# Optimization experiments

Measured on AMD Instinct MI355X. Metric: run time of the kernel, lower is better.

## Reference

```python
import jax, jax.numpy as jnp
import numpy as np

IN_DIM = 64
B, C, H, W = 4, IN_DIM, 64, 64
KEY_CH = IN_DIM // 8  # softmax scale channel count (as in torch code)


def conv1x1(x, w, b):
    # x: [B,C,H,W], w: [O,C], b: [O] -> [B,O,H,W]
    return jnp.einsum('bchw,oc->bohw', x, w) + b[None, :, None, None]


def setup_inputs() -> dict:
    key = jax.random.key(0)
    ks = jax.random.split(key, 24)
    s = 0.05
    d16, d4 = IN_DIM // 16, IN_DIM // 4
    inp = {
        'input1': jax.random.normal(ks[0], (B, C, H, W), jnp.float32),
        'input2': jax.random.normal(ks[1], (B, C, H, W), jnp.float32),
        'wq1': jax.random.normal(ks[2], (d16, C), jnp.float32) * s,
        'bq1': jax.random.normal(ks[3], (d16,), jnp.float32) * s,
        'wq2': jax.random.normal(ks[4], (d16, C), jnp.float32) * s,
        'bq2': jax.random.normal(ks[5], (d16,), jnp.float32) * s,
        'wq3': jax.random.normal(ks[6], (d16, C), jnp.float32) * s,
        'bq3': jax.random.normal(ks[7], (d16,), jnp.float32) * s,
        'wq4': jax.random.normal(ks[8], (d16, C), jnp.float32) * s,
        'bq4': jax.random.normal(ks[9], (d16,), jnp.float32) * s,
        'wk': jax.random.normal(ks[10], (d4, C), jnp.float32) * s,
        'bk': jax.random.normal(ks[11], (d4,), jnp.float32) * s,
        'wv': jax.random.normal(ks[12], (C, C), jnp.float32) * s,
        'bv': jax.random.normal(ks[13], (C,), jnp.float32) * s,
        'wk2': jax.random.normal(ks[14], (d4, C), jnp.float32) * s,
        'bk2': jax.random.normal(ks[15], (d4,), jnp.float32) * s,
        'wv2': jax.random.normal(ks[16], (C, C), jnp.float32) * s,
        'bv2': jax.random.normal(ks[17], (C,), jnp.float32) * s,
        'gamma': jax.random.normal(ks[18], (1,), jnp.float32) * 0.1,
    }
    return inp


def _branch(q_in, feat, wk_, bk_, wv_, bv_, gamma, resid):
    b, c, h, w = feat.shape
    n = h * w
    scale = KEY_CH ** (-0.5)
    q = q_in.reshape(b, -1, n).transpose(0, 2, 1)            # [B,N,C/4]
    k = conv1x1(feat, wk_, bk_).reshape(b, -1, n)            # [B,C/4,N]
    attn = jax.nn.softmax(scale * jnp.einsum('bnd,bdm->bnm', q, k), axis=-1)  # [B,N,N]
    v = conv1x1(feat, wv_, bv_).reshape(b, c, n)             # [B,C,N]
    out = jnp.einsum('bcn,bmn->bcm', v, attn).reshape(b, c, h, w)
    return gamma[0] * out + resid


def reference(input1, input2, wq1, bq1, wq2, bq2, wq3, bq3, wq4, bq4,
              wk, bk, wv, bv, wk2, bk2, wv2, bv2, gamma):
    input3 = input1 + (input2 - input1) / 3
    input4 = input3 + (input2 - input1) / 3
    q1 = conv1x1(input1, wq1, bq1)
    q2 = conv1x1(input2, wq2, bq2)
    q3 = conv1x1(input3, wq3, bq3)
    q4 = conv1x1(input4, wq4, bq4)
    q_in1 = jnp.concatenate([q1, q3, q4, q2], axis=1)  # [B,C/4,H,W]
    q_in2 = jnp.concatenate([q2, q4, q3, q1], axis=1)
    out1 = _branch(q_in1, input1, wk, bk, wv, bv, gamma, input1)
    out2 = _branch(q_in2, input2, wk2, bk2, wv2, bv2, gamma, input2)
    return out1, out2
```

## Files before the change

kernel.cpp:

```cpp
#include <hip/hip_runtime.h>
#include <hip/hip_bf16.h>
#include <stdint.h>

typedef short bf16x8 __attribute__((ext_vector_type(8)));
typedef float f32x4  __attribute__((ext_vector_type(4)));
typedef float f32x16 __attribute__((ext_vector_type(16)));
typedef unsigned int u32;

#define N_SP 4096
#define QSCALE 0.5100697284f

__device__ inline unsigned short f2bf(float f) {
    unsigned u = __float_as_uint(f);
    u += 0x7fff + ((u >> 16) & 1);
    return (unsigned short)(u >> 16);
}
__device__ inline float bf2f(short s) {
    return __uint_as_float(((unsigned)(unsigned short)s) << 16);
}
__device__ inline u32 cvtpk_bf16(float lo, float hi) {
    u32 r;
    asm("v_cvt_pk_bf16_f32 %0, %1, %2" : "=v"(r) : "v"(lo), "v"(hi));
    return r;
}
__device__ inline void pl32swap(u32& a, u32& b) {
    asm volatile("v_permlane32_swap_b32 %0, %1" : "+v"(a), "+v"(b));
}


__global__ __launch_bounds__(256) void stage1_kernel(
    const float* __restrict__ in1, const float* __restrict__ in2,
    const float* __restrict__ wq1, const float* __restrict__ bq1,
    const float* __restrict__ wq2, const float* __restrict__ bq2,
    const float* __restrict__ wq3, const float* __restrict__ bq3,
    const float* __restrict__ wq4, const float* __restrict__ bq4,
    const float* __restrict__ wk,  const float* __restrict__ bk,
    const float* __restrict__ wv,  const float* __restrict__ bv,
    const float* __restrict__ wk2, const float* __restrict__ bk2,
    const float* __restrict__ wv2, const float* __restrict__ bv2,
    unsigned short* __restrict__ Qs, unsigned short* __restrict__ Ks,
    unsigned short* __restrict__ Vs)
{
    __shared__ unsigned short w1h[16][64];
    __shared__ unsigned short w2h[16][64];
    __shared__ unsigned short wkh[16][64];
    __shared__ unsigned short wvh[64][64];
    __shared__ float qb[16], kbb[16], vbb[64];

    const int bid = blockIdx.x;
    const int br = bid & 7;
    const int ntl = bid >> 3;
    const int b = br >> 1, rr = br & 1;
    const int tid = threadIdx.x;

    const float* wqs[4]; const float* bqs[4]; float c1s[4], c2s[4];
    if (rr == 0) {
        wqs[0]=wq1; bqs[0]=bq1; c1s[0]=1.f;       c2s[0]=0.f;
        wqs[1]=wq3; bqs[1]=bq3; c1s[1]=2.f/3.f;   c2s[1]=1.f/3.f;
        wqs[2]=wq4; bqs[2]=bq4; c1s[2]=1.f/3.f;   c2s[2]=2.f/3.f;
        wqs[3]=wq2; bqs[3]=bq2; c1s[3]=0.f;       c2s[3]=1.f;
    } else {
        wqs[0]=wq2; bqs[0]=bq2; c1s[0]=0.f;       c2s[0]=1.f;
        wqs[1]=wq4; bqs[1]=bq4; c1s[1]=1.f/3.f;   c2s[1]=2.f/3.f;
        wqs[2]=wq3; bqs[2]=bq3; c1s[2]=2.f/3.f;   c2s[2]=1.f/3.f;
        wqs[3]=wq1; bqs[3]=bq1; c1s[3]=1.f;       c2s[3]=0.f;
    }
    const float* wkp = rr ? wk2 : wk;  const float* bkp = rr ? bk2 : bk;
    const float* wvp = rr ? wv2 : wv;  const float* bvp = rr ? bv2 : bv;

    for (int e = tid; e < 1024; e += 256) {
        int g = e >> 8;
        int h = e >> 6;
        int ch = e & 63;
        float wq_ = wqs[g][e & 255];
        w1h[h][ch] = f2bf(c1s[g] * wq_ * QSCALE);
        w2h[h][ch] = f2bf(c2s[g] * wq_ * QSCALE);
        wkh[h][ch] = f2bf(wkp[e]);
    }
    for (int e = tid; e < 4096; e += 256) wvh[e >> 6][e & 63] = f2bf(wvp[e]);
    if (tid < 16) { qb[tid] = bqs[tid >> 2][tid & 3] * QSCALE; kbb[tid] = bkp[tid]; }
    if (tid < 64) vbb[tid] = bvp[tid];
    __syncthreads();

    const int nl = tid & 31;
    const int og = tid >> 5;
    const int n = ntl * 32 + nl;
    const float* x1p = in1 + (size_t)b * 64 * N_SP + n;
    const float* x2p = in2 + (size_t)b * 64 * N_SP + n;
    const float* xfp = rr ? x2p : x1p;

    if (og < 2) {
        float acc[8];
        #pragma unroll
        for (int o = 0; o < 8; o++) acc[o] = qb[og * 8 + o];
        for (int g = 0; g < 8; g++) {
            float x1v[8], x2v[8];
            #pragma unroll
            for (int cc = 0; cc < 8; cc++) {
                x1v[cc] = x1p[(size_t)(g * 8 + cc) * N_SP];
                x2v[cc] = x2p[(size_t)(g * 8 + cc) * N_SP];
            }
            #pragma unroll
            for (int o = 0; o < 8; o++) {
                bf16x8 w1v = *(const bf16x8*)(&w1h[og * 8 + o][g * 8]);
                bf16x8 w2v = *(const bf16x8*)(&w2h[og * 8 + o][g * 8]);
                #pragma unroll
                for (int cc = 0; cc < 8; cc++)
                    acc[o] += bf2f(w1v[cc]) * x1v[cc] + bf2f(w2v[cc]) * x2v[cc];
            }
        }
        bf16x8 qv;
        #pragma unroll
        for (int o = 0; o < 8; o++) qv[o] = (short)f2bf(acc[o]);
        *(bf16x8*)(Qs + (size_t)br * 65536 + ntl * 512 + og * 256 + nl * 8) = qv;
    } else if (og < 4) {
        const int dg = og - 2;
        float acc[8];
        #pragma unroll
        for (int o = 0; o < 8; o++) acc[o] = kbb[dg * 8 + o];
        for (int g = 0; g < 8; g++) {
            float xfv[8];
            #pragma unroll
            for (int cc = 0; cc < 8; cc++) xfv[cc] = xfp[(size_t)(g * 8 + cc) * N_SP];
            #pragma unroll
            for (int o = 0; o < 8; o++) {
                bf16x8 wkv = *(const bf16x8*)(&wkh[dg * 8 + o][g * 8]);
                #pragma unroll
                for (int cc = 0; cc < 8; cc++)
                    acc[o] += bf2f(wkv[cc]) * xfv[cc];
            }
        }
        bf16x8 kv;
        #pragma unroll
        for (int o = 0; o < 8; o++) kv[o] = (short)f2bf(acc[o]);
        *(bf16x8*)(Ks + (size_t)br * 65536 + ntl * 512 + nl * 16 + dg * 8) = kv;
    } else {
        const int cg = og - 4;
        float acc[16];
        #pragma unroll
        for (int j = 0; j < 16; j++) acc[j] = vbb[cg * 16 + j];
        for (int g = 0; g < 8; g++) {
            float xfv[8];
            #pragma unroll
            for (int cc = 0; cc < 8; cc++) xfv[cc] = xfp[(size_t)(g * 8 + cc) * N_SP];
            #pragma unroll
            for (int j = 0; j < 16; j++) {
                bf16x8 wvv = *(const bf16x8*)(&wvh[cg * 16 + j][g * 8]);
                #pragma unroll
                for (int cc = 0; cc < 8; cc++)
                    acc[j] += bf2f(wvv[cc]) * xfv[cc];
            }
        }
        size_t basen = (size_t)br * 262144 + (size_t)(n >> 5) * 2048 +
                       (size_t)((n >> 4) & 1) * 1024 + (size_t)((n >> 3) & 1) * 256 +
                       (n & 7);
        #pragma unroll
        for (int j = 0; j < 16; j++) {
            int c = cg * 16 + j;
            Vs[basen + (c >> 5) * 512 + (c & 31) * 8] = f2bf(acc[j]);
        }
    }
}

__global__ __launch_bounds__(256, 4) void attn_kernel(
    const unsigned short* __restrict__ Qs, const unsigned short* __restrict__ Ks,
    const unsigned short* __restrict__ Vs,
    const float* __restrict__ in1, const float* __restrict__ in2,
    const float* __restrict__ gamma_p, float* __restrict__ out)
{
    __shared__ float accb[4][64][33];
    __shared__ float rsl[4][32];
    __shared__ float invl[32];

    const int bid = blockIdx.x;
    const int br = bid & 7;
    const int qt = bid >> 3;
    const int b = br >> 1, rr = br & 1;
    const int tid = threadIdx.x;
    const int ks = tid >> 6;
    const int l = tid & 63;
    const int q31 = l & 31, hi = l >> 5;

    const unsigned short* Qb = Qs + (size_t)br * 65536;
    const unsigned short* Kb = Ks + (size_t)br * 65536;
    const unsigned short* Vb = Vs + (size_t)br * 262144;

    const bf16x8 aq = *(const bf16x8*)(Qb + qt * 512 + l * 8);

    f32x16 accA = {0,0,0,0,0,0,0,0,0,0,0,0,0,0,0,0};
    f32x16 accB = {0,0,0,0,0,0,0,0,0,0,0,0,0,0,0,0};
    float rsum = 0.f;

    const int koff = q31 * 16 + hi * 8;

    bf16x8 kf[2];
    bf16x8 vf[2][4];
    {
        const unsigned short* kp = Kb + (size_t)(ks * 32) * 512;
        const unsigned short* vp = Vb + (size_t)(ks * 32) * 2048;
        kf[0] = *(const bf16x8*)(kp + koff);
        #pragma unroll
        for (int j = 0; j < 4; j++) vf[0][j] = *(const bf16x8*)(vp + j * 512 + l * 8);
    }

    #pragma unroll
    for (int t = 0; t < 32; ++t) {
        const int cur = t & 1, nxt = cur ^ 1;
        const int tn = (t < 31) ? t + 1 : 31;
        {
            const unsigned short* kpn = Kb + (size_t)(ks * 32 + tn) * 512;
            const unsigned short* vpn = Vb + (size_t)(ks * 32 + tn) * 2048;
            kf[nxt] = *(const bf16x8*)(kpn + koff);
            #pragma unroll
            for (int j = 0; j < 4; j++) vf[nxt][j] = *(const bf16x8*)(vpn + j * 512 + l * 8);
        }

        const f32x16 z16 = {0,0,0,0,0,0,0,0,0,0,0,0,0,0,0,0};
        f32x16 s = __builtin_amdgcn_mfma_f32_32x32x16_bf16(kf[cur], aq, z16, 0, 0, 0);

        float p[16];
        #pragma unroll
        for (int r2 = 0; r2 < 16; ++r2) {
            p[r2] = exp2f(s[r2]);
            rsum += p[r2];
        }

        u32 a0 = cvtpk_bf16(p[0], p[1]);   u32 a2 = cvtpk_bf16(p[4], p[5]);
        pl32swap(a0, a2);
        u32 a1 = cvtpk_bf16(p[2], p[3]);   u32 a3 = cvtpk_bf16(p[6], p[7]);
        pl32swap(a1, a3);
        u32 c0 = cvtpk_bf16(p[8], p[9]);   u32 c2 = cvtpk_bf16(p[12], p[13]);
        pl32swap(c0, c2);
        u32 c1 = cvtpk_bf16(p[10], p[11]); u32 c3 = cvtpk_bf16(p[14], p[15]);
        pl32swap(c1, c3);

        union U { u32 w[4]; bf16x8 v; };
        U u0; u0.w[0] = a0; u0.w[1] = a1; u0.w[2] = a2; u0.w[3] = a3;
        U u1; u1.w[0] = c0; u1.w[1] = c1; u1.w[2] = c2; u1.w[3] = c3;

        accA = __builtin_amdgcn_mfma_f32_32x32x16_bf16(u0.v, vf[cur][0], accA, 0, 0, 0);
        accB = __builtin_amdgcn_mfma_f32_32x32x16_bf16(u0.v, vf[cur][1], accB, 0, 0, 0);
        accA = __builtin_amdgcn_mfma_f32_32x32x16_bf16(u1.v, vf[cur][2], accA, 0, 0, 0);
        accB = __builtin_amdgcn_mfma_f32_32x32x16_bf16(u1.v, vf[cur][3], accB, 0, 0, 0);
    }

    rsum += __shfl_xor(rsum, 32, 64);
    if (l < 32) rsl[ks][l] = rsum;

    #pragma unroll
    for (int r2 = 0; r2 < 16; ++r2) {
        int qrow = (r2 & 3) + 8 * (r2 >> 2) + 4 * hi;
        accb[ks][q31][qrow]      = accA[r2];
        accb[ks][32 + q31][qrow] = accB[r2];
    }
    __syncthreads();

    if (tid < 32)
        invl[tid] = 1.0f / (rsl[0][tid] + rsl[1][tid] + rsl[2][tid] + rsl[3][tid]);
    __syncthreads();

    const float g = gamma_p[0];
    const int c = tid >> 2, mg = tid & 3;
    const float* fp = (rr ? in2 : in1) + (size_t)b * 64 * N_SP + (size_t)c * N_SP +
                      qt * 32 + mg * 8;
    float* op = out + (size_t)rr * (4ull * 64 * N_SP) + (size_t)b * 64 * N_SP +
                (size_t)c * N_SP + qt * 32 + mg * 8;

    float ov[8];
    #pragma unroll
    for (int i = 0; i < 8; i++) {
        int q = mg * 8 + i;
        ov[i] = (accb[0][c][q] + accb[1][c][q] + accb[2][c][q] + accb[3][c][q]) * invl[q];
    }
    f32x4 f0 = *(const f32x4*)fp;
    f32x4 f1 = *(const f32x4*)(fp + 4);
    f32x4 o0, o1;
    #pragma unroll
    for (int i = 0; i < 4; i++) {
        o0[i] = g * ov[i]     + f0[i];
        o1[i] = g * ov[4 + i] + f1[i];
    }
    *(f32x4*)op = o0;
    *(f32x4*)(op + 4) = o1;
}

extern "C" void kernel_launch(void* const* d_in, const int* in_sizes, int n_in,
                              void* d_out, int out_size, void* d_ws, size_t ws_size,
                              hipStream_t stream) {
    const float* in1 = (const float*)d_in[0];
    const float* in2 = (const float*)d_in[1];
    const float* wq1 = (const float*)d_in[2];  const float* bq1 = (const float*)d_in[3];
    const float* wq2 = (const float*)d_in[4];  const float* bq2 = (const float*)d_in[5];
    const float* wq3 = (const float*)d_in[6];  const float* bq3 = (const float*)d_in[7];
    const float* wq4 = (const float*)d_in[8];  const float* bq4 = (const float*)d_in[9];
    const float* wk  = (const float*)d_in[10]; const float* bk  = (const float*)d_in[11];
    const float* wv  = (const float*)d_in[12]; const float* bv  = (const float*)d_in[13];
    const float* wk2 = (const float*)d_in[14]; const float* bk2 = (const float*)d_in[15];
    const float* wv2 = (const float*)d_in[16]; const float* bv2 = (const float*)d_in[17];
    const float* gamma_p = (const float*)d_in[18];

    unsigned short* Qs = (unsigned short*)d_ws;
    unsigned short* Ks = Qs + (size_t)8 * 65536;
    unsigned short* Vs = Ks + (size_t)8 * 65536;

    stage1_kernel<<<dim3(1024), 256, 0, stream>>>(in1, in2, wq1, bq1, wq2, bq2,
                                                  wq3, bq3, wq4, bq4, wk, bk, wv, bv,
                                                  wk2, bk2, wv2, bv2, Qs, Ks, Vs);
    attn_kernel<<<dim3(1024), 256, 0, stream>>>(Qs, Ks, Vs, in1, in2, gamma_p,
                                                (float*)d_out);
}
```

Before: 150.7 us.

## Restructure attention: 4 query tiles per block sharing LDS-staged K/V pipeline

Measured after the change: 196.4 us. +30.3%, slower.

```diff
diff --git a/kernel.cpp b/kernel.cpp
--- a/kernel.cpp
+++ b/kernel.cpp
@@ -15,9 +15,6 @@
     u += 0x7fff + ((u >> 16) & 1);
     return (unsigned short)(u >> 16);
 }
-__device__ inline float bf2f(short s) {
-    return __uint_as_float(((unsigned)(unsigned short)s) << 16);
-}
 __device__ inline u32 cvtpk_bf16(float lo, float hi) {
     u32 r;
     asm("v_cvt_pk_bf16_f32 %0, %1, %2" : "=v"(r) : "v"(lo), "v"(hi));
@@ -26,6 +23,13 @@
 __device__ inline void pl32swap(u32& a, u32& b) {
     asm volatile("v_permlane32_swap_b32 %0, %1" : "+v"(a), "+v"(b));
 }
+__device__ inline void gl_lds16(const void* g, void* l) {
+    __builtin_amdgcn_global_load_lds(
+        (const __attribute__((address_space(1))) unsigned int*)g,
+        (__attribute__((address_space(3))) unsigned int*)l, 16, 0, 0);
+}
+
+union U { u32 w[4]; bf16x8 v; };
 
 
 __global__ __launch_bounds__(256) void stage1_kernel(
@@ -41,10 +45,10 @@
     unsigned short* __restrict__ Qs, unsigned short* __restrict__ Ks,
     unsigned short* __restrict__ Vs)
 {
-    __shared__ unsigned short w1h[16][64];
-    __shared__ unsigned short w2h[16][64];
-    __shared__ unsigned short wkh[16][64];
-    __shared__ unsigned short wvh[64][64];
+    __shared__ float w1f[16][64];
+    __shared__ float w2f[16][64];
+    __shared__ float wkf[16][64];
+    __shared__ float wvf[64][64];
     __shared__ float qb[16], kbb[16], vbb[64];
 
     const int bid = blockIdx.x;
@@ -73,11 +77,11 @@
         int h = e >> 6;
         int ch = e & 63;
         float wq_ = wqs[g][e & 255];
-        w1h[h][ch] = f2bf(c1s[g] * wq_ * QSCALE);
-        w2h[h][ch] = f2bf(c2s[g] * wq_ * QSCALE);
-        wkh[h][ch] = f2bf(wkp[e]);
-    }
-    for (int e = tid; e < 4096; e += 256) wvh[e >> 6][e & 63] = f2bf(wvp[e]);
+        w1f[h][ch] = c1s[g] * wq_ * QSCALE;
+        w2f[h][ch] = c2s[g] * wq_ * QSCALE;
+        wkf[h][ch] = wkp[e];
+    }
+    for (int e = tid; e < 4096; e += 256) wvf[e >> 6][e & 63] = wvp[e];
     if (tid < 16) { qb[tid] = bqs[tid >> 2][tid & 3] * QSCALE; kbb[tid] = bkp[tid]; }
     if (tid < 64) vbb[tid] = bvp[tid];
     __syncthreads();
@@ -102,11 +106,14 @@
             }
             #pragma unroll
             for (int o = 0; o < 8; o++) {
-                bf16x8 w1v = *(const bf16x8*)(&w1h[og * 8 + o][g * 8]);
-                bf16x8 w2v = *(const bf16x8*)(&w2h[og * 8 + o][g * 8]);
+                const f32x4* w1p = (const f32x4*)&w1f[og * 8 + o][g * 8];
+                const f32x4* w2p = (const f32x4*)&w2f[og * 8 + o][g * 8];
+                f32x4 wa = w1p[0], wb = w1p[1], wc = w2p[0], wd = w2p[1];
                 #pragma unroll
-                for (int cc = 0; cc < 8; cc++)
-                    acc[o] += bf2f(w1v[cc]) * x1v[cc] + bf2f(w2v[cc]) * x2v[cc];
+                for (int cc = 0; cc < 4; cc++) {
+                    acc[o] += wa[cc] * x1v[cc]     + wc[cc] * x2v[cc];
+                    acc[o] += wb[cc] * x1v[4 + cc] + wd[cc] * x2v[4 + cc];
+                }
             }
         }
         bf16x8 qv;
@@ -124,16 +131,19 @@
             for (int cc = 0; cc < 8; cc++) xfv[cc] = xfp[(size_t)(g * 8 + cc) * N_SP];
             #pragma unroll
             for (int o = 0; o < 8; o++) {
-                bf16x8 wkv = *(const bf16x8*)(&wkh[dg * 8 + o][g * 8]);
+                const f32x4* wkq = (const f32x4*)&wkf[dg * 8 + o][g * 8];
+                f32x4 wa = wkq[0], wb = wkq[1];
                 #pragma unroll
-                for (int cc = 0; cc < 8; cc++)
-                    acc[o] += bf2f(wkv[cc]) * xfv[cc];
+                for (int cc = 0; cc < 4; cc++) {
+                    acc[o] += wa[cc] * xfv[cc];
+                    acc[o] += wb[cc] * xfv[4 + cc];
+                }
             }
         }
         bf16x8 kv;
         #pragma unroll
         for (int o = 0; o < 8; o++) kv[o] = (short)f2bf(acc[o]);
-        *(bf16x8*)(Ks + (size_t)br * 65536 + ntl * 512 + nl * 16 + dg * 8) = kv;
+        *(bf16x8*)(Ks + (size_t)br * 65536 + ntl * 512 + dg * 256 + nl * 8) = kv;
     } else {
         const int cg = og - 4;
         float acc[16];
@@ -145,143 +155,145 @@
             for (int cc = 0; cc < 8; cc++) xfv[cc] = xfp[(size_t)(g * 8 + cc) * N_SP];
             #pragma unroll
             for (int j = 0; j < 16; j++) {
-                bf16x8 wvv = *(const bf16x8*)(&wvh[cg * 16 + j][g * 8]);
+                const f32x4* wvq = (const f32x4*)&wvf[cg * 16 + j][g * 8];
+                f32x4 wa = wvq[0], wb = wvq[1];
                 #pragma unroll
-                for (int cc = 0; cc < 8; cc++)
-                    acc[j] += bf2f(wvv[cc]) * xfv[cc];
+                for (int cc = 0; cc < 4; cc++) {
+                    acc[j] += wa[cc] * xfv[cc];
+                    acc[j] += wb[cc] * xfv[4 + cc];
+                }
             }
         }
-        size_t basen = (size_t)br * 262144 + (size_t)(n >> 5) * 2048 +
-                       (size_t)((n >> 4) & 1) * 1024 + (size_t)((n >> 3) & 1) * 256 +
-                       (n & 7);
+        const int key5 = n & 31, kt = key5 >> 4, keyr = key5 & 15;
+        const int hi_ = keyr >> 3, j_ = keyr & 7;
+        size_t vbase = (size_t)br * 262144 + (size_t)(n >> 5) * 2048 +
+                       (size_t)hi_ * 256 + j_;
         #pragma unroll
         for (int j = 0; j < 16; j++) {
             int c = cg * 16 + j;
-            Vs[basen + (c >> 5) * 512 + (c & 31) * 8] = f2bf(acc[j]);
+            Vs[vbase + (size_t)((kt * 2 + (c >> 5)) * 512 + (c & 31) * 8)] = f2bf(acc[j]);
         }
     }
 }
 
-__global__ __launch_bounds__(256, 4) void attn_kernel(
+#define STAGE(T) do {                                                          \
+    int nt_ = (T); int bi_ = nt_ & 3;                                          \
+    gl_lds16(Vb + (size_t)nt_ * 2048 + tid * 8, &lsV[bi_][tid * 8]);           \
+    if (w == 0) gl_lds16(Kb + (size_t)nt_ * 512 + l * 8, &lsK[bi_][l * 8]);    \
+} while (0)
+
+#define FRAG_READ(S, BI) do {                                                  \
+    int bi_ = (BI);                                                            \
+    const short* kp_ = &lsK[bi_][l * 8];                                       \
+    const short* vp_ = &lsV[bi_][l * 8];                                       \
+    fk##S  = *(const bf16x8*)kp_;                                              \
+    fv0##S = *(const bf16x8*)(vp_);                                            \
+    fv1##S = *(const bf16x8*)(vp_ + 512);                                      \
+    fv2##S = *(const bf16x8*)(vp_ + 1024);                                     \
+    fv3##S = *(const bf16x8*)(vp_ + 1536);                                     \
+} while (0)
+
+#define COMPUTE(S) do {                                                        \
+    f32x16 s_ = __builtin_amdgcn_mfma_f32_32x32x16_bf16(fk##S, aq, z16, 0, 0, 0); \
+    float p_[16];                                                              \
+    _Pragma("unroll")                                                          \
+    for (int r_ = 0; r_ < 16; ++r_) p_[r_] = __builtin_amdgcn_exp2f(s_[r_]);   \
+    u32 a0 = cvtpk_bf16(p_[0], p_[1]),  a2 = cvtpk_bf16(p_[4], p_[5]);         \
+    pl32swap(a0, a2);                                                          \
+    u32 a1 = cvtpk_bf16(p_[2], p_[3]),  a3 = cvtpk_bf16(p_[6], p_[7]);         \
+    pl32swap(a1, a3);                                                          \
+    u32 c0 = cvtpk_bf16(p_[8], p_[9]),  c2 = cvtpk_bf16(p_[12], p_[13]);       \
+    pl32swap(c0, c2);                                                          \
+    u32 c1 = cvtpk_bf16(p_[10], p_[11]), c3 = cvtpk_bf16(p_[14], p_[15]);      \
+    pl32swap(c1, c3);                                                          \
+    U u0_, u1_;                                                                \
+    u0_.w[0] = a0; u0_.w[1] = a1; u0_.w[2] = a2; u0_.w[3] = a3;                \
+    u1_.w[0] = c0; u1_.w[1] = c1; u1_.w[2] = c2; u1_.w[3] = c3;                \
+    acc0 = __builtin_amdgcn_mfma_f32_32x32x16_bf16(fv0##S, u0_.v, acc0, 0, 0, 0); \
+    acc1 = __builtin_amdgcn_mfma_f32_32x32x16_bf16(fv1##S, u0_.v, acc1, 0, 0, 0); \
+    acc0 = __builtin_amdgcn_mfma_f32_32x32x16_bf16(fv2##S, u1_.v, acc0, 0, 0, 0); \
+    acc1 = __builtin_amdgcn_mfma_f32_32x32x16_bf16(fv3##S, u1_.v, acc1, 0, 0, 0); \
+    accR = __builtin_amdgcn_mfma_f32_32x32x16_bf16(ones, u0_.v, accR, 0, 0, 0);   \
+    accR = __builtin_amdgcn_mfma_f32_32x32x16_bf16(ones, u1_.v, accR, 0, 0, 0);   \
+} while (0)
+
+#define SYNC(TT) do {                                                          \
+    if ((TT) < 125) {                                                          \
+        if (w == 0) asm volatile("s_waitcnt vmcnt(2) lgkmcnt(0)" ::: "memory");\
+        else        asm volatile("s_waitcnt vmcnt(1) lgkmcnt(0)" ::: "memory");\
+    } else {                                                                   \
+        asm volatile("s_waitcnt vmcnt(0) lgkmcnt(0)" ::: "memory");            \
+    }                                                                          \
+    __builtin_amdgcn_s_barrier();                                              \
+} while (0)
+
+__global__ __launch_bounds__(256, 1) void attn_kernel(
     const unsigned short* __restrict__ Qs, const unsigned short* __restrict__ Ks,
     const unsigned short* __restrict__ Vs,
     const float* __restrict__ in1, const float* __restrict__ in2,
     const float* __restrict__ gamma_p, float* __restrict__ out)
 {
-    __shared__ float accb[4][64][33];
-    __shared__ float rsl[4][32];
-    __shared__ float invl[32];
+    __shared__ short lsK[4][512];
+    __shared__ short lsV[4][2048];
 
     const int bid = blockIdx.x;
     const int br = bid & 7;
-    const int qt = bid >> 3;
+    const int qtg = bid >> 3;
     const int b = br >> 1, rr = br & 1;
     const int tid = threadIdx.x;
-    const int ks = tid >> 6;
+    const int w = tid >> 6;
     const int l = tid & 63;
     const int q31 = l & 31, hi = l >> 5;
+    const int qt = qtg * 4 + w;
 
     const unsigned short* Qb = Qs + (size_t)br * 65536;
     const unsigned short* Kb = Ks + (size_t)br * 65536;
     const unsigned short* Vb = Vs + (size_t)br * 262144;
 
     const bf16x8 aq = *(const bf16x8*)(Qb + qt * 512 + l * 8);
-
-    f32x16 accA = {0,0,0,0,0,0,0,0,0,0,0,0,0,0,0,0};
-    f32x16 accB = {0,0,0,0,0,0,0,0,0,0,0,0,0,0,0,0};
-    float rsum = 0.f;
-
-    const int koff = q31 * 16 + hi * 8;
-
-    bf16x8 kf[2];
-    bf16x8 vf[2][4];
-    {
-        const unsigned short* kp = Kb + (size_t)(ks * 32) * 512;
-        const unsigned short* vp = Vb + (size_t)(ks * 32) * 2048;
-        kf[0] = *(const bf16x8*)(kp + koff);
-        #pragma unroll
-        for (int j = 0; j < 4; j++) vf[0][j] = *(const bf16x8*)(vp + j * 512 + l * 8);
-    }
-
+    bf16x8 ones;
     #pragma unroll
-    for (int t = 0; t < 32; ++t) {
-        const int cur = t & 1, nxt = cur ^ 1;
-        const int tn = (t < 31) ? t + 1 : 31;
-        {
-            const unsigned short* kpn = Kb + (size_t)(ks * 32 + tn) * 512;
-            const unsigned short* vpn = Vb + (size_t)(ks * 32 + tn) * 2048;
-            kf[nxt] = *(const bf16x8*)(kpn + koff);
-            #pragma unroll
-            for (int j = 0; j < 4; j++) vf[nxt][j] = *(const bf16x8*)(vpn + j * 512 + l * 8);
-        }
-
-        const f32x16 z16 = {0,0,0,0,0,0,0,0,0,0,0,0,0,0,0,0};
-        f32x16 s = __builtin_amdgcn_mfma_f32_32x32x16_bf16(kf[cur], aq, z16, 0, 0, 0);
-
-        float p[16];
-        #pragma unroll
-        for (int r2 = 0; r2 < 16; ++r2) {
-            p[r2] = exp2f(s[r2]);
-            rsum += p[r2];
-        }
-
-        u32 a0 = cvtpk_bf16(p[0], p[1]);   u32 a2 = cvtpk_bf16(p[4], p[5]);
-        pl32swap(a0, a2);
-        u32 a1 = cvtpk_bf16(p[2], p[3]);   u32 a3 = cvtpk_bf16(p[6], p[7]);
-        pl32swap(a1, a3);
-        u32 c0 = cvtpk_bf16(p[8], p[9]);   u32 c2 = cvtpk_bf16(p[12], p[13]);
-        pl32swap(c0, c2);
-        u32 c1 = cvtpk_bf16(p[10], p[11]); u32 c3 = cvtpk_bf16(p[14], p[15]);
-        pl32swap(c1, c3);
-
-        union U { u32 w[4]; bf16x8 v; };
-        U u0; u0.w[0] = a0; u0.w[1] = a1; u0.w[2] = a2; u0.w[3] = a3;
-        U u1; u1.w[0] = c0; u1.w[1] = c1; u1.w[2] = c2; u1.w[3] = c3;
-
-        accA = __builtin_amdgcn_mfma_f32_32x32x16_bf16(u0.v, vf[cur][0], accA, 0, 0, 0);
-        accB = __builtin_amdgcn_mfma_f32_32x32x16_bf16(u0.v, vf[cur][1], accB, 0, 0, 0);
-        accA = __builtin_amdgcn_mfma_f32_32x32x16_bf16(u1.v, vf[cur][2], accA, 0, 0, 0);
-        accB = __builtin_amdgcn_mfma_f32_32x32x16_bf16(u1.v, vf[cur][3], accB, 0, 0, 0);
-    }
-
-    rsum += __shfl_xor(rsum, 32, 64);
-    if (l < 32) rsl[ks][l] = rsum;
+    for (int j = 0; j < 8; j++) ones[j] = (short)0x3F80;
+    const f32x16 z16 = {0,0,0,0,0,0,0,0,0,0,0,0,0,0,0,0};
+
+    f32x16 acc0 = z16;
+    f32x16 acc1 = z16;
+    f32x16 accR = z16;
+
+    bf16x8 fk0, fv00, fv10, fv20, fv30;
+    bf16x8 fk1, fv01, fv11, fv21, fv31;
+
+    STAGE(0); STAGE(1); STAGE(2);
+    if (w == 0) asm volatile("s_waitcnt vmcnt(2)" ::: "memory");
+    else        asm volatile("s_waitcnt vmcnt(1)" ::: "memory");
+    __builtin_amdgcn_s_barrier();
+    FRAG_READ(0, 0);
+
+    for (int t = 0; t < 128; t += 2) {
+        if (t + 3 < 128) STAGE(t + 3);
+        FRAG_READ(1, (t + 1) & 3);
+        COMPUTE(0);
+        SYNC(t);
+        if (t + 4 < 128) STAGE(t + 4);
+        if (t + 2 < 128) FRAG_READ(0, (t + 2) & 3);
+        COMPUTE(1);
+        if (t + 2 < 128) SYNC(t + 1);
+    }
+
+    const float g = gamma_p[0];
+    const float inv = 1.0f / accR[0];
+    const float* featp = (rr ? in2 : in1) + (size_t)b * 64 * N_SP;
+    float* outp = out + (size_t)rr * (4ull * 64 * N_SP) + (size_t)b * 64 * N_SP;
+    const int m = qt * 32 + q31;
 
     #pragma unroll
-    for (int r2 = 0; r2 < 16; ++r2) {
-        int qrow = (r2 & 3) + 8 * (r2 >> 2) + 4 * hi;
-        accb[ks][q31][qrow]      = accA[r2];
-        accb[ks][32 + q31][qrow] = accB[r2];
-    }
-    __syncthreads();
-
-    if (tid < 32)
-        invl[tid] = 1.0f / (rsl[0][tid] + rsl[1][tid] + rsl[2][tid] + rsl[3][tid]);
-    __syncthreads();
-
-    const float g = gamma_p[0];
-    const int c = tid >> 2, mg = tid & 3;
-    const float* fp = (rr ? in2 : in1) + (size_t)b * 64 * N_SP + (size_t)c * N_SP +
-                      qt * 32 + mg * 8;
-    float* op = out + (size_t)rr * (4ull * 64 * N_SP) + (size_t)b * 64 * N_SP +
-                (size_t)c * N_SP + qt * 32 + mg * 8;
-
-    float ov[8];
-    #pragma unroll
-    for (int i = 0; i < 8; i++) {
-        int q = mg * 8 + i;
-        ov[i] = (accb[0][c][q] + accb[1][c][q] + accb[2][c][q] + accb[3][c][q]) * invl[q];
-    }
-    f32x4 f0 = *(const f32x4*)fp;
-    f32x4 f1 = *(const f32x4*)(fp + 4);
-    f32x4 o0, o1;
-    #pragma unroll
-    for (int i = 0; i < 4; i++) {
-        o0[i] = g * ov[i]     + f0[i];
-        o1[i] = g * ov[4 + i] + f1[i];
-    }
-    *(f32x4*)op = o0;
-    *(f32x4*)(op + 4) = o1;
+    for (int r = 0; r < 16; r++) {
+        int c = (r & 3) + 8 * (r >> 2) + 4 * hi;
+        size_t o1 = (size_t)c * N_SP + m;
+        size_t o2 = (size_t)(c + 32) * N_SP + m;
+        outp[o1] = g * (acc0[r] * inv) + featp[o1];
+        outp[o2] = g * (acc1[r] * inv) + featp[o2];
+    }
 }
 
 extern "C" void kernel_launch(void* const* d_in, const int* in_sizes, int n_in,
@@ -306,6 +318,6 @@
     stage1_kernel<<<dim3(1024), 256, 0, stream>>>(in1, in2, wq1, bq1, wq2, bq2,
                                                   wq3, bq3, wq4, bq4, wk, bk, wv, bv,
                                                   wk2, bk2, wv2, bv2, Qs, Ks, Vs);
-    attn_kernel<<<dim3(1024), 256, 0, stream>>>(Qs, Ks, Vs, in1, in2, gamma_p,
-                                                (float*)d_out);
-}
+    attn_kernel<<<dim3(256), 256, 0, stream>>>(Qs, Ks, Vs, in1, in2, gamma_p,
+                                               (float*)d_out);
+}
```
